# Performance work log

Hardware: AMD Instinct MI355X
Metric: run time of the kernel (lower is better)

Reference implementation:

```python
import jax, jax.numpy as jnp
import numpy as np

W = 64   # window_size
S = 1    # window_stride
H = 4    # n_head
D = 64   # head_size


def setup_inputs() -> dict:
    key = jax.random.key(0)
    ks = jax.random.split(key, 6)
    B, T, C = 2, 2048, 256
    x = jax.random.normal(ks[0], (B, T, C), jnp.float32)
    w_kqv = jax.random.normal(ks[1], (3 * H * D, C), jnp.float32) * 0.05
    w_out = jax.random.normal(ks[2], (C, H * D), jnp.float32) * 0.05
    b_out = jax.random.normal(ks[3], (C,), jnp.float32) * 0.05
    q_pos = jax.random.normal(ks[4], (W, H, D), jnp.float32) * 0.05
    v_pos = jax.random.normal(ks[5], (W, H, D), jnp.float32) * 0.05
    return dict(x=x, w_kqv=w_kqv, w_out=w_out, b_out=b_out, q_pos=q_pos, v_pos=v_pos)


def reference(x, w_kqv, w_out, b_out, q_pos, v_pos):
    B, T, C = x.shape
    # qkv projection: (B, T, 3, H, D)
    kqv = (x @ w_kqv.T).reshape(B, T, 3, H, D)
    # zero-pad W*S steps at the front of time (matches F.pad before as_strided)
    xp = jnp.pad(kqv, ((0, 0), (W * S, 0), (0, 0), (0, 0), (0, 0)))
    Tq = T - S  # output rows after the [:, S:] slice
    # window slot w of output row t' reads padded time t' + S*(w+1)
    # (= original token t' + S - S*(W - w), i.e. tokens t-S, t-2S, ..., t-W*S)
    idx = jnp.arange(Tq)[:, None] + S * (jnp.arange(W)[None, :] + 1)  # (Tq, W)
    win = xp[:, idx]  # (B, Tq, W, 3, H, D)
    tk = win[:, :, :, 0]
    tq = win[:, :, :, 1]
    tv = win[:, :, :, 2]
    # per-slot dot (both k and q come from the same strided window, as in the source)
    wei = jnp.einsum('btwhd,btwhd->btwh', tk, tq)
    wei = wei + jnp.einsum('whd,btwhd->btwh', q_pos, tq)  # relative query bias
    wei = wei * (D ** -0.5)  # scale applied AFTER the relative add, as in source
    # flipped-tril causal mask: row i keeps slots w >= W-1-i (all-true for i >= W)
    valid = jnp.arange(W)[None, :] >= (W - 1 - jnp.arange(Tq)[:, None])  # (Tq, W)
    wei = jnp.where(valid[None, :, :, None], wei, -jnp.inf)
    wei = jax.nn.softmax(wei, axis=2)  # softmax over window dim (dim=-2 in torch)
    # dropout omitted (inference / rate 0)
    out = jnp.einsum('btwh,btwhd->bthd', wei, tv)
    out = out + jnp.einsum('btwh,whd->bthd', wei, v_pos)  # relative value bias
    out = out.reshape(B, Tq, H * D)
    out = jnp.pad(out, ((0, 0), (S, 0), (0, 0)))  # re-pad the first S rows with zeros
    y = out @ w_out.T + b_out
    return (y, wei)
```

## Files before the change

kernel.cpp:

```cpp
#include <hip/hip_runtime.h>
#include <hip/hip_bf16.h>
#include <math.h>

#define BB 2
#define TT 2048
#define CC 256
#define HH 4
#define DD 64
#define WW 64
#define TQ 2047
#define N_KQV 768

typedef __attribute__((ext_vector_type(8))) short bf16x8;
typedef __attribute__((ext_vector_type(4))) float f32x4;

__device__ inline short f2bf(float x) {
    unsigned u = __float_as_uint(x);
    u += 0x7FFF + ((u >> 16) & 1);
    return (short)(u >> 16);
}
__device__ inline float bf2f(short s) {
    return __uint_as_float(((unsigned)(unsigned short)s) << 16);
}
__device__ inline bf16x8 cvt8(float4 a, float4 b) {
    bf16x8 r;
    r[0] = f2bf(a.x); r[1] = f2bf(a.y); r[2] = f2bf(a.z); r[3] = f2bf(a.w);
    r[4] = f2bf(b.x); r[5] = f2bf(b.y); r[6] = f2bf(b.z); r[7] = f2bf(b.w);
    return r;
}

template<bool ABF, int BM, int BN, int WR, int WC, bool ZROW, bool BIAS, bool CBF>
__global__ __launch_bounds__(256)
void gemm_mfma(const void* __restrict__ Av, const float* __restrict__ Bm,
               const float* __restrict__ bias, void* __restrict__ Cv,
               int M, int N, int K) {
    constexpr int BK = 64;
    constexpr int LDA = BK + 8;
    constexpr int MR = BM / (WR * 16);
    constexpr int NR = BN / (WC * 16);
    __shared__ short As[BM][LDA];
    __shared__ short Bs[BN][LDA];

    const int tid = threadIdx.x;
    const int m0 = blockIdx.x * BM, n0 = blockIdx.y * BN;
    const int wv = tid >> 6, lane = tid & 63;
    const int wr = wv / WC, wc = wv % WC;
    const int col = lane & 15, kg = lane >> 4;

    f32x4 acc[MR][NR];
#pragma unroll
    for (int i = 0; i < MR; ++i)
#pragma unroll
        for (int j = 0; j < NR; ++j) acc[i][j] = (f32x4){0.f, 0.f, 0.f, 0.f};

    for (int k0 = 0; k0 < K; k0 += BK) {
#pragma unroll
        for (int it = 0; it < BM / 32; ++it) {
            int fi = tid + it * 256;
            int r = fi >> 3, c8 = (fi & 7) << 3;
            int gr = m0 + r;
            bf16x8 sv;
            if (ZROW && ((gr & (TT - 1)) == 0)) {
                sv = (bf16x8){0, 0, 0, 0, 0, 0, 0, 0};
            } else if constexpr (ABF) {
                sv = *reinterpret_cast<const bf16x8*>(
                    (const short*)Av + (size_t)gr * K + k0 + c8);
            } else {
                const float* ap = (const float*)Av + (size_t)gr * K + k0 + c8;
                float4 v0 = *reinterpret_cast<const float4*>(ap);
                float4 v1 = *reinterpret_cast<const float4*>(ap + 4);
                sv = cvt8(v0, v1);
            }
            *reinterpret_cast<bf16x8*>(&As[r][c8]) = sv;
        }
#pragma unroll
        for (int it = 0; it < BN / 32; ++it) {
            int fi = tid + it * 256;
            int r = fi >> 3, c8 = (fi & 7) << 3;
            const float* bp = Bm + (size_t)(n0 + r) * K + k0 + c8;
            float4 v0 = *reinterpret_cast<const float4*>(bp);
            float4 v1 = *reinterpret_cast<const float4*>(bp + 4);
            *reinterpret_cast<bf16x8*>(&Bs[r][c8]) = cvt8(v0, v1);
        }
        __syncthreads();

#pragma unroll
        for (int kk = 0; kk < 2; ++kk) {
            bf16x8 af[MR], bfr[NR];
#pragma unroll
            for (int i = 0; i < MR; ++i)
                af[i] = *reinterpret_cast<const bf16x8*>(
                    &As[wr * MR * 16 + i * 16 + col][kk * 32 + kg * 8]);
#pragma unroll
            for (int j = 0; j < NR; ++j)
                bfr[j] = *reinterpret_cast<const bf16x8*>(
                    &Bs[wc * NR * 16 + j * 16 + col][kk * 32 + kg * 8]);
#pragma unroll
            for (int i = 0; i < MR; ++i)
#pragma unroll
                for (int j = 0; j < NR; ++j)
                    acc[i][j] = __builtin_amdgcn_mfma_f32_16x16x32_bf16(
                        af[i], bfr[j], acc[i][j], 0, 0, 0);
        }
        __syncthreads();
    }

#pragma unroll
    for (int i = 0; i < MR; ++i) {
#pragma unroll
        for (int j = 0; j < NR; ++j) {
#pragma unroll
            for (int r = 0; r < 4; ++r) {
                int m = m0 + wr * MR * 16 + i * 16 + kg * 4 + r;
                int n = n0 + wc * NR * 16 + j * 16 + col;
                float v = acc[i][j][r];
                if (BIAS) v += bias[n];
                if constexpr (CBF)
                    ((short*)Cv)[(size_t)m * N + n] = f2bf(v);
                else
                    ((float*)Cv)[(size_t)m * N + n] = v;
            }
        }
    }
}

__global__ __launch_bounds__(256)
void attn_fused(const short* __restrict__ kqvb, const float* __restrict__ q_pos,
                const float* __restrict__ v_pos, float* __restrict__ wei_out,
                short* __restrict__ attnSb) {
    __shared__ __align__(16) short lds[40192];
    float* ldsf = reinterpret_cast<float*>(lds);
    short* QS = lds;
    short* PP = lds;
    short* PD = lds + 6656;
    short* PS = lds + 11264;
    short* VT = lds + 15872;
    short* VP = lds + 26624;
    float* PT = ldsf + 15616;
    float* SB = ldsf + 15616;
    float* DQ = ldsf + 19968;

    const int tid  = threadIdx.x;
    const int wv   = tid >> 6;
    const int lane = tid & 63;
    const int col  = lane & 15;
    const int kg   = lane >> 4;
    const int bid  = blockIdx.x;
    const int tile = bid & 31;
    const int h    = (bid >> 5) & 3;
    const int b    = bid >> 7;
    const int t0   = tile * 64;
    const int j0   = t0 - 63;

#pragma unroll
    for (int it = 0; it < 4; ++it) {
        int fi = tid + it * 256;
        int r = fi >> 3, c8 = (fi & 7) << 3;
        int j = j0 + r;
        bf16x8 qv = (bf16x8){0,0,0,0,0,0,0,0};
        bf16x8 kv = (bf16x8){0,0,0,0,0,0,0,0};
        if (j >= 0 && j < TT) {
            const short* base = kqvb + ((size_t)(b * TT + j)) * N_KQV + h * DD + c8;
            kv = *reinterpret_cast<const bf16x8*>(base);
            qv = *reinterpret_cast<const bf16x8*>(base + 256);
        }
        *reinterpret_cast<bf16x8*>(&QS[r * 72 + c8]) = qv;
        float s = 0.f;
#pragma unroll
        for (int q = 0; q < 8; ++q) s += bf2f(kv[q]) * bf2f(qv[q]);
        PT[r * 9 + (fi & 7)] = s;
    }
#pragma unroll
    for (int it = 0; it < 2; ++it) {
        int fi = tid + it * 256;
        int r = fi >> 3, c8 = (fi & 7) << 3;
        const float* pp = q_pos + (size_t)(r * HH + h) * DD + c8;
        float4 v0 = *reinterpret_cast<const float4*>(pp);
        float4 v1 = *reinterpret_cast<const float4*>(pp + 4);
        *reinterpret_cast<bf16x8*>(&PS[r * 72 + c8]) = cvt8(v0, v1);
    }
#pragma unroll
    for (int it = 0; it < 5; ++it) {
        int fi = tid + it * 256;
        int r = fi >> 3, c8 = (fi & 7) << 3;
        int j = j0 + r;
        bf16x8 v = (bf16x8){0,0,0,0,0,0,0,0};
        if (j >= 0 && j < TT)
            v = *reinterpret_cast<const bf16x8*>(
                kqvb + ((size_t)(b * TT + j)) * N_KQV + 512 + h * DD + c8);
#pragma unroll
        for (int q = 0; q < 8; ++q) VT[(c8 + q) * 168 + r] = v[q];
    }
#pragma unroll
    for (int it = 0; it < 2; ++it) {
        int fi = tid + it * 256;
        int r = fi >> 3, c8 = (fi & 7) << 3;
        const float* pp = v_pos + (size_t)(r * HH + h) * DD + c8;
        float4 v0 = *reinterpret_cast<const float4*>(pp);
        float4 v1 = *reinterpret_cast<const float4*>(pp + 4);
        bf16x8 v = cvt8(v0, v1);
#pragma unroll
        for (int q = 0; q < 8; ++q) VP[(c8 + q) * 72 + r] = v[q];
    }
    __syncthreads();

    f32x4 qacc[2][4];
#pragma unroll
    for (int mi = 0; mi < 2; ++mi)
#pragma unroll
        for (int n = 0; n < 4; ++n) qacc[mi][n] = (f32x4){0.f, 0.f, 0.f, 0.f};

#pragma unroll
    for (int ks = 0; ks < 2; ++ks) {
        bf16x8 af[2], bfr[4];
#pragma unroll
        for (int mi = 0; mi < 2; ++mi)
            af[mi] = *reinterpret_cast<const bf16x8*>(
                &QS[(wv * 32 + mi * 16 + col) * 72 + ks * 32 + kg * 8]);
#pragma unroll
        for (int n = 0; n < 4; ++n)
            bfr[n] = *reinterpret_cast<const bf16x8*>(
                &PS[(n * 16 + col) * 72 + ks * 32 + kg * 8]);
#pragma unroll
        for (int mi = 0; mi < 2; ++mi)
#pragma unroll
            for (int n = 0; n < 4; ++n)
                qacc[mi][n] = __builtin_amdgcn_mfma_f32_16x16x32_bf16(
                    af[mi], bfr[n], qacc[mi][n], 0, 0, 0);
    }
    if (tid < 128) {
        float s = 0.f;
#pragma unroll
        for (int g = 0; g < 8; ++g) s += PT[tid * 9 + g];
        DQ[tid] = s;
    }
    __syncthreads();

    {
        unsigned int* pz = reinterpret_cast<unsigned int*>(lds);
#pragma unroll
        for (int i = 0; i < 22; ++i) pz[tid + i * 256] = 0u;
    }
#pragma unroll
    for (int mi = 0; mi < 2; ++mi) {
#pragma unroll
        for (int n = 0; n < 4; ++n) {
            int w = n * 16 + col;
#pragma unroll
            for (int r = 0; r < 4; ++r) {
                int jl = wv * 32 + mi * 16 + kg * 4 + r;
                int it_ = jl - w;
                if (it_ >= 0 && it_ < 64) SB[it_ * 68 + w] = qacc[mi][n][r];
            }
        }
    }
    __syncthreads();

    const int rs = lane >> 4;
    const int wg = lane & 15;
    const bool edge = (t0 == 0);
#pragma unroll
    for (int i4 = 0; i4 < 4; ++i4) {
        int i = wv * 16 + i4 * 4 + rs;
        int t = t0 + i;
        f32x4 sv = *reinterpret_cast<const f32x4*>(&SB[i * 68 + wg * 4]);
        float s[4];
#pragma unroll
        for (int q = 0; q < 4; ++q) {
            int w = wg * 4 + q;
            s[q] = (sv[q] + DQ[i + w]) * 0.125f;
            if (edge && (i - 63 + w) < 0) s[q] = -INFINITY;
        }
        float m = fmaxf(fmaxf(s[0], s[1]), fmaxf(s[2], s[3]));
#pragma unroll
        for (int off = 8; off; off >>= 1) m = fmaxf(m, __shfl_xor(m, off));
        float p[4], sum = 0.f;
#pragma unroll
        for (int q = 0; q < 4; ++q) { p[q] = __expf(s[q] - m); sum += p[q]; }
#pragma unroll
        for (int off = 8; off; off >>= 1) sum += __shfl_xor(sum, off);
        float inv = 1.f / sum;
        int il = i4 * 4 + rs;
#pragma unroll
        for (int q = 0; q < 4; ++q) {
            int w = wg * 4 + q;
            float wei = p[q] * inv;
            if (t < TQ)
                wei_out[(((size_t)b * TQ + t) * WW + w) * HH + h] = wei;
            short wb = f2bf(wei);
            PD[wv * 1152 + il * 72 + w] = wb;
            PP[wv * 1664 + il * 104 + il + w] = wb;
        }
    }
    __syncthreads();

    f32x4 pacc[4];
#pragma unroll
    for (int dt = 0; dt < 4; ++dt) pacc[dt] = (f32x4){0.f, 0.f, 0.f, 0.f};
    const int jbase = wv * 16;
#pragma unroll
    for (int ks = 0; ks < 3; ++ks) {
        bf16x8 afrag = *reinterpret_cast<const bf16x8*>(
            &PP[wv * 1664 + col * 104 + ks * 32 + kg * 8]);
#pragma unroll
        for (int dt = 0; dt < 4; ++dt) {
            bf16x8 bfrag = *reinterpret_cast<const bf16x8*>(
                &VT[(dt * 16 + col) * 168 + jbase + ks * 32 + kg * 8]);
            pacc[dt] = __builtin_amdgcn_mfma_f32_16x16x32_bf16(afrag, bfrag, pacc[dt], 0, 0, 0);
        }
    }
#pragma unroll
    for (int ks = 0; ks < 2; ++ks) {
        bf16x8 afrag = *reinterpret_cast<const bf16x8*>(
            &PD[wv * 1152 + col * 72 + ks * 32 + kg * 8]);
#pragma unroll
        for (int dt = 0; dt < 4; ++dt) {
            bf16x8 bfrag = *reinterpret_cast<const bf16x8*>(
                &VP[(dt * 16 + col) * 72 + ks * 32 + kg * 8]);
            pacc[dt] = __builtin_amdgcn_mfma_f32_16x16x32_bf16(afrag, bfrag, pacc[dt], 0, 0, 0);
        }
    }

    const int ta = t0 + wv * 16;
#pragma unroll
    for (int dt = 0; dt < 4; ++dt) {
#pragma unroll
        for (int r = 0; r < 4; ++r) {
            int t = ta + kg * 4 + r;
            if (t < TQ)
                attnSb[((size_t)(b * TT) + t + 1) * CC + h * DD + dt * 16 + col] =
                    f2bf(pacc[dt][r]);
        }
    }
}

extern "C" void kernel_launch(void* const* d_in, const int* in_sizes, int n_in,
                              void* d_out, int out_size, void* d_ws, size_t ws_size,
                              hipStream_t stream) {
    const float* x     = (const float*)d_in[0];
    const float* w_kqv = (const float*)d_in[1];
    const float* w_out = (const float*)d_in[2];
    const float* b_out = (const float*)d_in[3];
    const float* q_pos = (const float*)d_in[4];
    const float* v_pos = (const float*)d_in[5];

    float* y   = (float*)d_out;
    float* wei = (float*)d_out + (size_t)BB * TT * CC;

    short* kqvb   = (short*)d_ws;
    short* attnSb = kqvb + (size_t)BB * TT * N_KQV;

    gemm_mfma<false, 64, 96, 2, 2, false, false, true>
        <<<dim3((BB * TT) / 64, N_KQV / 96), 256, 0, stream>>>(
            x, w_kqv, nullptr, kqvb, BB * TT, N_KQV, CC);

    attn_fused<<<BB * HH * 32, 256, 0, stream>>>(kqvb, q_pos, v_pos, wei, attnSb);

    gemm_mfma<true, 32, 64, 2, 2, true, true, false>
        <<<dim3((BB * TT) / 32, CC / 64), 256, 0, stream>>>(
            attnSb, w_out, b_out, y, BB * TT, CC, CC);
}
```

Measured before the change: 34.94 us.

## Shrink attention tiles to 16 rows and pre-convert weights in QKV GEMM

The attention kernel now processes 16 query rows per block instead of 64, so it launches four times as many blocks with much smaller LDS use and higher occupancy. It reads Q fragments straight from global memory instead of staging them. Extra blocks in the first GEMM convert w_out, q_pos and a transposed v_pos to bf16 once into workspace. The attention kernel and the output GEMM then load bf16 data directly without converting per block. In exchange, the V and Q windows overlap between blocks (79 rows loaded per 16 outputs), which adds redundant global reads.

Result: slower. 45.18 us (+29.3%).

```diff
diff --git a/kernel.cpp b/kernel.cpp
--- a/kernel.cpp
+++ b/kernel.cpp
@@ -29,11 +29,16 @@
     return r;
 }
 
-template<bool ABF, int BM, int BN, int WR, int WC, bool ZROW, bool BIAS, bool CBF>
+template<bool ABF, bool BBF, int BM, int BN, int WR, int WC,
+         bool ZROW, bool BIAS, bool CBF, bool CONV>
 __global__ __launch_bounds__(256)
-void gemm_mfma(const void* __restrict__ Av, const float* __restrict__ Bm,
+void gemm_mfma(const void* __restrict__ Av, const void* __restrict__ Bv,
                const float* __restrict__ bias, void* __restrict__ Cv,
-               int M, int N, int K) {
+               int M, int N, int K,
+               const float* __restrict__ qposf, const float* __restrict__ vposf,
+               const float* __restrict__ woutf,
+               short* __restrict__ qposb, short* __restrict__ vposTb,
+               short* __restrict__ woutb) {
     constexpr int BK = 64;
     constexpr int LDA = BK + 8;
     constexpr int MR = BM / (WR * 16);
@@ -42,6 +47,27 @@
     __shared__ short Bs[BN][LDA];
 
     const int tid = threadIdx.x;
+
+    if (CONV && (int)blockIdx.x == (int)gridDim.x - 1) {
+        const int base = blockIdx.y * 12288;
+#pragma unroll
+        for (int i = 0; i < 48; ++i) {
+            int e = base + i * 256 + tid;
+            if (e < 65536) {
+                woutb[e] = f2bf(woutf[e]);
+            } else if (e < 81920) {
+                int e2 = e - 65536;
+                int h = e2 >> 12, r = e2 & 4095, w = r >> 6, d = r & 63;
+                qposb[e2] = f2bf(qposf[(w * HH + h) * DD + d]);
+            } else {
+                int e3 = e - 81920;
+                int h = e3 >> 12, r = e3 & 4095, d = r >> 6, w = r & 63;
+                vposTb[e3] = f2bf(vposf[(w * HH + h) * DD + d]);
+            }
+        }
+        return;
+    }
+
     const int m0 = blockIdx.x * BM, n0 = blockIdx.y * BN;
     const int wv = tid >> 6, lane = tid & 63;
     const int wr = wv / WC, wc = wv % WC;
@@ -77,10 +103,17 @@
         for (int it = 0; it < BN / 32; ++it) {
             int fi = tid + it * 256;
             int r = fi >> 3, c8 = (fi & 7) << 3;
-            const float* bp = Bm + (size_t)(n0 + r) * K + k0 + c8;
-            float4 v0 = *reinterpret_cast<const float4*>(bp);
-            float4 v1 = *reinterpret_cast<const float4*>(bp + 4);
-            *reinterpret_cast<bf16x8*>(&Bs[r][c8]) = cvt8(v0, v1);
+            bf16x8 sv;
+            if constexpr (BBF) {
+                sv = *reinterpret_cast<const bf16x8*>(
+                    (const short*)Bv + (size_t)(n0 + r) * K + k0 + c8);
+            } else {
+                const float* bp = (const float*)Bv + (size_t)(n0 + r) * K + k0 + c8;
+                float4 v0 = *reinterpret_cast<const float4*>(bp);
+                float4 v1 = *reinterpret_cast<const float4*>(bp + 4);
+                sv = cvt8(v0, v1);
+            }
+            *reinterpret_cast<bf16x8*>(&Bs[r][c8]) = sv;
         }
         __syncthreads();
 
@@ -125,20 +158,14 @@
 }
 
 __global__ __launch_bounds__(256)
-void attn_fused(const short* __restrict__ kqvb, const float* __restrict__ q_pos,
-                const float* __restrict__ v_pos, float* __restrict__ wei_out,
+void attn_fused(const short* __restrict__ kqvb, const short* __restrict__ qposb,
+                const short* __restrict__ vposTb, float* __restrict__ wei_out,
                 short* __restrict__ attnSb) {
-    __shared__ __align__(16) short lds[40192];
-    float* ldsf = reinterpret_cast<float*>(lds);
-    short* QS = lds;
-    short* PP = lds;
-    short* PD = lds + 6656;
-    short* PS = lds + 11264;
-    short* VT = lds + 15872;
-    short* VP = lds + 26624;
-    float* PT = ldsf + 15616;
-    float* SB = ldsf + 15616;
-    float* DQ = ldsf + 19968;
+    __shared__ __align__(16) short VT[64 * 104];
+    __shared__ __align__(16) short PP[16 * 104];
+    __shared__ __align__(16) short PD[16 * 72];
+    __shared__ float SB[16 * 68];
+    __shared__ float DQ[80];
 
     const int tid  = threadIdx.x;
     const int wv   = tid >> 6;
@@ -146,141 +173,116 @@
     const int col  = lane & 15;
     const int kg   = lane >> 4;
     const int bid  = blockIdx.x;
-    const int tile = bid & 31;
-    const int h    = (bid >> 5) & 3;
-    const int b    = bid >> 7;
-    const int t0   = tile * 64;
+    const int tile = bid & 127;
+    const int h    = (bid >> 7) & 3;
+    const int b    = bid >> 9;
+    const int t0   = tile * 16;
     const int j0   = t0 - 63;
 
-#pragma unroll
-    for (int it = 0; it < 4; ++it) {
+    {
+        unsigned int* pz = reinterpret_cast<unsigned int*>(PP);
+#pragma unroll
+        for (int i = 0; i < 4; ++i) {
+            int fi = tid + i * 256;
+            if (fi < 832) pz[fi] = 0u;
+        }
+    }
+
+    if (tid < 158) {
+        int row = tid >> 1, half = tid & 1;
+        int j = j0 + row;
+        float s = 0.f;
+        if (j >= 0) {
+            const short* kp = kqvb + ((size_t)(b * TT + j)) * N_KQV + h * DD + half * 32;
+            const short* qp = kp + 256;
+#pragma unroll
+            for (int c = 0; c < 32; c += 8) {
+                bf16x8 kv = *reinterpret_cast<const bf16x8*>(kp + c);
+                bf16x8 qv = *reinterpret_cast<const bf16x8*>(qp + c);
+#pragma unroll
+                for (int q = 0; q < 8; ++q) s += bf2f(kv[q]) * bf2f(qv[q]);
+            }
+        }
+        s += __shfl_xor(s, 1);
+        if (half == 0) DQ[row] = s;
+    }
+
+#pragma unroll
+    for (int it = 0; it < 3; ++it) {
         int fi = tid + it * 256;
-        int r = fi >> 3, c8 = (fi & 7) << 3;
+        int r = fi >> 3, c = fi & 7, c8 = c << 3;
         int j = j0 + r;
-        bf16x8 qv = (bf16x8){0,0,0,0,0,0,0,0};
-        bf16x8 kv = (bf16x8){0,0,0,0,0,0,0,0};
-        if (j >= 0 && j < TT) {
-            const short* base = kqvb + ((size_t)(b * TT + j)) * N_KQV + h * DD + c8;
-            kv = *reinterpret_cast<const bf16x8*>(base);
-            qv = *reinterpret_cast<const bf16x8*>(base + 256);
-        }
-        *reinterpret_cast<bf16x8*>(&QS[r * 72 + c8]) = qv;
-        float s = 0.f;
-#pragma unroll
-        for (int q = 0; q < 8; ++q) s += bf2f(kv[q]) * bf2f(qv[q]);
-        PT[r * 9 + (fi & 7)] = s;
-    }
-#pragma unroll
-    for (int it = 0; it < 2; ++it) {
-        int fi = tid + it * 256;
-        int r = fi >> 3, c8 = (fi & 7) << 3;
-        const float* pp = q_pos + (size_t)(r * HH + h) * DD + c8;
-        float4 v0 = *reinterpret_cast<const float4*>(pp);
-        float4 v1 = *reinterpret_cast<const float4*>(pp + 4);
-        *reinterpret_cast<bf16x8*>(&PS[r * 72 + c8]) = cvt8(v0, v1);
-    }
-#pragma unroll
-    for (int it = 0; it < 5; ++it) {
-        int fi = tid + it * 256;
-        int r = fi >> 3, c8 = (fi & 7) << 3;
-        int j = j0 + r;
-        bf16x8 v = (bf16x8){0,0,0,0,0,0,0,0};
-        if (j >= 0 && j < TT)
+        bf16x8 v = (bf16x8){0, 0, 0, 0, 0, 0, 0, 0};
+        if (r < 79 && j >= 0)
             v = *reinterpret_cast<const bf16x8*>(
                 kqvb + ((size_t)(b * TT + j)) * N_KQV + 512 + h * DD + c8);
 #pragma unroll
-        for (int q = 0; q < 8; ++q) VT[(c8 + q) * 168 + r] = v[q];
-    }
-#pragma unroll
-    for (int it = 0; it < 2; ++it) {
-        int fi = tid + it * 256;
-        int r = fi >> 3, c8 = (fi & 7) << 3;
-        const float* pp = v_pos + (size_t)(r * HH + h) * DD + c8;
-        float4 v0 = *reinterpret_cast<const float4*>(pp);
-        float4 v1 = *reinterpret_cast<const float4*>(pp + 4);
-        bf16x8 v = cvt8(v0, v1);
-#pragma unroll
-        for (int q = 0; q < 8; ++q) VP[(c8 + q) * 72 + r] = v[q];
-    }
-    __syncthreads();
-
-    f32x4 qacc[2][4];
-#pragma unroll
-    for (int mi = 0; mi < 2; ++mi)
-#pragma unroll
-        for (int n = 0; n < 4; ++n) qacc[mi][n] = (f32x4){0.f, 0.f, 0.f, 0.f};
-
-#pragma unroll
-    for (int ks = 0; ks < 2; ++ks) {
-        bf16x8 af[2], bfr[4];
-#pragma unroll
-        for (int mi = 0; mi < 2; ++mi)
-            af[mi] = *reinterpret_cast<const bf16x8*>(
-                &QS[(wv * 32 + mi * 16 + col) * 72 + ks * 32 + kg * 8]);
-#pragma unroll
-        for (int n = 0; n < 4; ++n)
-            bfr[n] = *reinterpret_cast<const bf16x8*>(
-                &PS[(n * 16 + col) * 72 + ks * 32 + kg * 8]);
-#pragma unroll
-        for (int mi = 0; mi < 2; ++mi)
-#pragma unroll
-            for (int n = 0; n < 4; ++n)
-                qacc[mi][n] = __builtin_amdgcn_mfma_f32_16x16x32_bf16(
-                    af[mi], bfr[n], qacc[mi][n], 0, 0, 0);
-    }
-    if (tid < 128) {
-        float s = 0.f;
-#pragma unroll
-        for (int g = 0; g < 8; ++g) s += PT[tid * 9 + g];
-        DQ[tid] = s;
-    }
-    __syncthreads();
-
-    {
-        unsigned int* pz = reinterpret_cast<unsigned int*>(lds);
-#pragma unroll
-        for (int i = 0; i < 22; ++i) pz[tid + i * 256] = 0u;
-    }
-#pragma unroll
-    for (int mi = 0; mi < 2; ++mi) {
+        for (int q0 = 0; q0 < 8; ++q0) {
+            int qp = (q0 + c) & 7;
+            VT[(c8 + qp) * 104 + r] = v[qp];
+        }
+    }
+
+    f32x4 qa[2][4];
+#pragma unroll
+    for (int im = 0; im < 2; ++im)
+#pragma unroll
+        for (int n = 0; n < 4; ++n) qa[im][n] = (f32x4){0.f, 0.f, 0.f, 0.f};
+    const int nmt = (wv == 0) ? 2 : 1;
+    for (int im = 0; im < nmt; ++im) {
+        int mt = im ? 4 : wv;
+#pragma unroll
+        for (int ks = 0; ks < 2; ++ks) {
+            int jr = j0 + mt * 16 + col;
+            bf16x8 af = (bf16x8){0, 0, 0, 0, 0, 0, 0, 0};
+            if (jr >= 0)
+                af = *reinterpret_cast<const bf16x8*>(
+                    kqvb + ((size_t)(b * TT + jr)) * N_KQV + 256 + h * DD + ks * 32 + kg * 8);
+#pragma unroll
+            for (int n = 0; n < 4; ++n) {
+                bf16x8 bfr = *reinterpret_cast<const bf16x8*>(
+                    qposb + h * 4096 + (n * 16 + col) * 64 + ks * 32 + kg * 8);
+                qa[im][n] = __builtin_amdgcn_mfma_f32_16x16x32_bf16(af, bfr, qa[im][n], 0, 0, 0);
+            }
+        }
+    }
+    for (int im = 0; im < nmt; ++im) {
+        int mt = im ? 4 : wv;
 #pragma unroll
         for (int n = 0; n < 4; ++n) {
             int w = n * 16 + col;
 #pragma unroll
             for (int r = 0; r < 4; ++r) {
-                int jl = wv * 32 + mi * 16 + kg * 4 + r;
-                int it_ = jl - w;
-                if (it_ >= 0 && it_ < 64) SB[it_ * 68 + w] = qacc[mi][n][r];
+                int jl = mt * 16 + kg * 4 + r;
+                int il = jl - w;
+                if (il >= 0 && il < 16) SB[il * 68 + w] = qa[im][n][r];
             }
         }
     }
     __syncthreads();
 
-    const int rs = lane >> 4;
-    const int wg = lane & 15;
-    const bool edge = (t0 == 0);
-#pragma unroll
-    for (int i4 = 0; i4 < 4; ++i4) {
-        int i = wv * 16 + i4 * 4 + rs;
-        int t = t0 + i;
-        f32x4 sv = *reinterpret_cast<const f32x4*>(&SB[i * 68 + wg * 4]);
-        float s[4];
+    {
+        const int row = wv * 4 + kg;
+        const int wg  = col;
+        const int t   = t0 + row;
+        f32x4 sv = *reinterpret_cast<const f32x4*>(&SB[row * 68 + wg * 4]);
+        float s4[4];
 #pragma unroll
         for (int q = 0; q < 4; ++q) {
             int w = wg * 4 + q;
-            s[q] = (sv[q] + DQ[i + w]) * 0.125f;
-            if (edge && (i - 63 + w) < 0) s[q] = -INFINITY;
-        }
-        float m = fmaxf(fmaxf(s[0], s[1]), fmaxf(s[2], s[3]));
+            float s = (sv[q] + DQ[row + w]) * 0.125f;
+            if (tile < 4 && (j0 + row + w) < 0) s = -INFINITY;
+            s4[q] = s;
+        }
+        float m = fmaxf(fmaxf(s4[0], s4[1]), fmaxf(s4[2], s4[3]));
 #pragma unroll
         for (int off = 8; off; off >>= 1) m = fmaxf(m, __shfl_xor(m, off));
         float p[4], sum = 0.f;
 #pragma unroll
-        for (int q = 0; q < 4; ++q) { p[q] = __expf(s[q] - m); sum += p[q]; }
+        for (int q = 0; q < 4; ++q) { p[q] = __expf(s4[q] - m); sum += p[q]; }
 #pragma unroll
         for (int off = 8; off; off >>= 1) sum += __shfl_xor(sum, off);
         float inv = 1.f / sum;
-        int il = i4 * 4 + rs;
 #pragma unroll
         for (int q = 0; q < 4; ++q) {
             int w = wg * 4 + q;
@@ -288,49 +290,32 @@
             if (t < TQ)
                 wei_out[(((size_t)b * TQ + t) * WW + w) * HH + h] = wei;
             short wb = f2bf(wei);
-            PD[wv * 1152 + il * 72 + w] = wb;
-            PP[wv * 1664 + il * 104 + il + w] = wb;
+            PD[row * 72 + w] = wb;
+            PP[row * 104 + row + w] = wb;
         }
     }
     __syncthreads();
 
-    f32x4 pacc[4];
-#pragma unroll
-    for (int dt = 0; dt < 4; ++dt) pacc[dt] = (f32x4){0.f, 0.f, 0.f, 0.f};
-    const int jbase = wv * 16;
+    f32x4 pa = (f32x4){0.f, 0.f, 0.f, 0.f};
 #pragma unroll
     for (int ks = 0; ks < 3; ++ks) {
-        bf16x8 afrag = *reinterpret_cast<const bf16x8*>(
-            &PP[wv * 1664 + col * 104 + ks * 32 + kg * 8]);
-#pragma unroll
-        for (int dt = 0; dt < 4; ++dt) {
-            bf16x8 bfrag = *reinterpret_cast<const bf16x8*>(
-                &VT[(dt * 16 + col) * 168 + jbase + ks * 32 + kg * 8]);
-            pacc[dt] = __builtin_amdgcn_mfma_f32_16x16x32_bf16(afrag, bfrag, pacc[dt], 0, 0, 0);
-        }
+        bf16x8 af = *reinterpret_cast<const bf16x8*>(&PP[col * 104 + ks * 32 + kg * 8]);
+        bf16x8 bfr = *reinterpret_cast<const bf16x8*>(
+            &VT[(wv * 16 + col) * 104 + ks * 32 + kg * 8]);
+        pa = __builtin_amdgcn_mfma_f32_16x16x32_bf16(af, bfr, pa, 0, 0, 0);
     }
 #pragma unroll
     for (int ks = 0; ks < 2; ++ks) {
-        bf16x8 afrag = *reinterpret_cast<const bf16x8*>(
-            &PD[wv * 1152 + col * 72 + ks * 32 + kg * 8]);
-#pragma unroll
-        for (int dt = 0; dt < 4; ++dt) {
-            bf16x8 bfrag = *reinterpret_cast<const bf16x8*>(
-                &VP[(dt * 16 + col) * 72 + ks * 32 + kg * 8]);
-            pacc[dt] = __builtin_amdgcn_mfma_f32_16x16x32_bf16(afrag, bfrag, pacc[dt], 0, 0, 0);
-        }
-    }
-
-    const int ta = t0 + wv * 16;
-#pragma unroll
-    for (int dt = 0; dt < 4; ++dt) {
-#pragma unroll
-        for (int r = 0; r < 4; ++r) {
-            int t = ta + kg * 4 + r;
-            if (t < TQ)
-                attnSb[((size_t)(b * TT) + t + 1) * CC + h * DD + dt * 16 + col] =
-                    f2bf(pacc[dt][r]);
-        }
+        bf16x8 af = *reinterpret_cast<const bf16x8*>(&PD[col * 72 + ks * 32 + kg * 8]);
+        bf16x8 bfr = *reinterpret_cast<const bf16x8*>(
+            vposTb + h * 4096 + (wv * 16 + col) * 64 + ks * 32 + kg * 8);
+        pa = __builtin_amdgcn_mfma_f32_16x16x32_bf16(af, bfr, pa, 0, 0, 0);
+    }
+#pragma unroll
+    for (int r = 0; r < 4; ++r) {
+        int t = t0 + kg * 4 + r;
+        if (t < TQ)
+            attnSb[((size_t)(b * TT) + t + 1) * CC + h * DD + wv * 16 + col] = f2bf(pa[r]);
     }
 }
 
@@ -348,15 +333,20 @@
     float* wei = (float*)d_out + (size_t)BB * TT * CC;
 
     short* kqvb   = (short*)d_ws;
-    short* attnSb = kqvb + (size_t)BB * TT * N_KQV;
-
-    gemm_mfma<false, 64, 96, 2, 2, false, false, true>
-        <<<dim3((BB * TT) / 64, N_KQV / 96), 256, 0, stream>>>(
-            x, w_kqv, nullptr, kqvb, BB * TT, N_KQV, CC);
-
-    attn_fused<<<BB * HH * 32, 256, 0, stream>>>(kqvb, q_pos, v_pos, wei, attnSb);
-
-    gemm_mfma<true, 32, 64, 2, 2, true, true, false>
+    short* woutb  = kqvb + (size_t)BB * TT * N_KQV;
+    short* qposb  = woutb + 65536;
+    short* vposTb = qposb + 16384;
+    short* attnSb = vposTb + 16384;
+
+    gemm_mfma<false, false, 64, 96, 2, 2, false, false, true, true>
+        <<<dim3((BB * TT) / 64 + 1, N_KQV / 96), 256, 0, stream>>>(
+            x, w_kqv, nullptr, kqvb, BB * TT, N_KQV, CC,
+            q_pos, v_pos, w_out, qposb, vposTb, woutb);
+
+    attn_fused<<<BB * HH * 128, 256, 0, stream>>>(kqvb, qposb, vposTb, wei, attnSb);
+
+    gemm_mfma<true, true, 32, 64, 2, 2, true, true, false, false>
         <<<dim3((BB * TT) / 32, CC / 64), 256, 0, stream>>>(
-            attnSb, w_out, b_out, y, BB * TT, CC, CC);
-}
+            attnSb, woutb, b_out, y, BB * TT, CC, CC,
+            nullptr, nullptr, nullptr, nullptr, nullptr, nullptr);
+}
```
